# Kernel optimization log

Hardware: AMD Instinct MI355X
Metric: run time of the kernel (lower is better)

The kernel has to match this reference:

```python
import jax, jax.numpy as jnp
import numpy as np

N = 4096
H = 512
NUM_HEADS = 8
HEAD_DIM = H // NUM_HEADS
NUM_SETS = 1365


def setup_inputs() -> dict:
    key = jax.random.key(0)
    ks = jax.random.split(key, 24)
    s = 1.0 / np.sqrt(H)
    def lin(i):
        W = jax.random.normal(ks[i], (H, H), dtype=jnp.float32) * s
        b = jnp.zeros((H,), dtype=jnp.float32)
        return W, b
    Ws, bs = lin(0)
    Wq1, bq1 = lin(1); Wk1, bk1 = lin(2); Wv1, bv1 = lin(3); Wo1, bo1 = lin(4)
    Wq2, bq2 = lin(5); Wk2, bk2 = lin(6); Wv2, bv2 = lin(7); Wo2, bo2 = lin(8)
    # beta init is zeros in the module; use small nonzero so attention path matters
    beta1 = jnp.array([0.1], dtype=jnp.float32)
    beta2 = jnp.array([0.1], dtype=jnp.float32)
    embeddings = jax.random.normal(ks[9], (N, H), dtype=jnp.float32)
    batch_indices = jnp.sort(jax.random.randint(ks[10], (N,), 0, NUM_SETS))
    return dict(embeddings=embeddings, batch_indices=batch_indices,
                Ws=Ws, bs=bs,
                Wq1=Wq1, bq1=bq1, Wk1=Wk1, bk1=bk1, Wv1=Wv1, bv1=bv1, Wo1=Wo1, bo1=bo1, beta1=beta1,
                Wq2=Wq2, bq2=bq2, Wk2=Wk2, bk2=bk2, Wv2=Wv2, bv2=bv2, Wo2=Wo2, bo2=bo2, beta2=beta2)


def _attn_layer(x, mask, Wq, bq, Wk, bk, Wv, bv, Wo, bo, beta):
    n = x.shape[0]
    q = (x @ Wq + bq).reshape(n, NUM_HEADS, HEAD_DIM)
    k = (x @ Wk + bk).reshape(n, NUM_HEADS, HEAD_DIM)
    v = (x @ Wv + bv).reshape(n, NUM_HEADS, HEAD_DIM)
    scores = jnp.einsum('nhd,mhd->hnm', q, k) / np.sqrt(HEAD_DIM).astype(np.float32)
    scores = jnp.where(mask[None, :, :], scores, -jnp.inf)
    w = jax.nn.softmax(scores, axis=-1)
    w = jnp.nan_to_num(w, nan=0.0)  # rows with no valid key -> 0 (matches torch nan_to_num)
    out = jnp.einsum('hnm,mhd->nhd', w, v).reshape(n, H)
    return beta * (out @ Wo + bo) + x


def reference(embeddings, batch_indices, Ws, bs,
              Wq1, bq1, Wk1, bk1, Wv1, bv1, Wo1, bo1, beta1,
              Wq2, bq2, Wk2, bk2, Wv2, bv2, Wo2, bo2, beta2):
    n = embeddings.shape[0]
    static_emb = jax.nn.relu(embeddings @ Ws + bs)
    same_set = batch_indices[:, None] == batch_indices[None, :]
    mask = same_set & ~jnp.eye(n, dtype=bool)
    dyn = _attn_layer(embeddings, mask, Wq1, bq1, Wk1, bk1, Wv1, bv1, Wo1, bo1, beta1)
    dyn = _attn_layer(dyn, mask, Wq2, bq2, Wk2, bk2, Wv2, bv2, Wo2, bo2, beta2)
    sq = (dyn - static_emb) ** 2
    seg_sum = jax.ops.segment_sum(sq, batch_indices, num_segments=NUM_SETS)
    cnt = jax.ops.segment_sum(jnp.ones((n,), dtype=sq.dtype), batch_indices, num_segments=NUM_SETS)
    return seg_sum / jnp.maximum(cnt, 1.0)[:, None]
```

## Files before the change

kernel.cpp:

```cpp
#include <hip/hip_runtime.h>
#include <hip/hip_bf16.h>
#include <math.h>
#include <stdint.h>

#define N_NODES   4096
#define HDIM      512
#define NUM_HEADS 8
#define HEAD_DIM  64
#define NUM_SETS  1365
#define KDIM      512

typedef __attribute__((ext_vector_type(8))) short bf16x8;
typedef __attribute__((ext_vector_type(4))) float f32x4;

__device__ inline unsigned short f2bfu(float x) {
    __hip_bfloat16 h = __float2bfloat16(x);
    return __builtin_bit_cast(unsigned short, h);
}
__device__ inline float bfu2f(unsigned short u) {
    unsigned v = (unsigned)u << 16;
    return __builtin_bit_cast(float, v);
}

__device__ inline void gload_lds16(const void* g, void* l) {
    __builtin_amdgcn_global_load_lds(
        (const __attribute__((address_space(1))) unsigned int*)g,
        (__attribute__((address_space(3))) unsigned int*)l,
        16, 0, 0);
}

__global__ __launch_bounds__(256) void prep_kernel(
        const float* W0, const float* W1, const float* W2, const float* W3,
        const float* W4, const float* W5, const float* W6, const float* W7,
        const float* W8, __hip_bfloat16* __restrict__ wt,
        const float* __restrict__ emb, __hip_bfloat16* __restrict__ embb,
        const int* __restrict__ batch,
        int* __restrict__ seg_s, int* __restrict__ seg_e) {
    const int bx = blockIdx.x;
    if (bx < 2304) {
        __shared__ float t[32][36];
        const int z = bx >> 8;
        const int tb = bx & 255;
        const float* W = z==0?W0:z==1?W1:z==2?W2:z==3?W3:z==4?W4:z==5?W5:z==6?W6:z==7?W7:W8;
        __hip_bfloat16* Wt = wt + (size_t)z * (512 * 512);
        const int bn = (tb & 15) * 32, bk = (tb >> 4) * 32;
        const int nx = threadIdx.x & 7, ky = threadIdx.x >> 3;
        *(float4*)&t[ky][nx * 4] = *(const float4*)&W[(size_t)(bk + ky) * 512 + bn + nx * 4];
        __syncthreads();
        const int r2 = threadIdx.x >> 3;
        const int ck = threadIdx.x & 7;
        uint2 p;
        p.x = (unsigned)f2bfu(t[ck * 4 + 0][r2]) | ((unsigned)f2bfu(t[ck * 4 + 1][r2]) << 16);
        p.y = (unsigned)f2bfu(t[ck * 4 + 2][r2]) | ((unsigned)f2bfu(t[ck * 4 + 3][r2]) << 16);
        *(uint2*)&Wt[(size_t)(bn + r2) * 512 + bk + ck * 4] = p;
    } else if (bx < 4352) {
        const int i = (bx - 2304) * 256 + threadIdx.x;
        float4 v = ((const float4*)emb)[i];
        uint2 p;
        p.x = (unsigned)f2bfu(v.x) | ((unsigned)f2bfu(v.y) << 16);
        p.y = (unsigned)f2bfu(v.z) | ((unsigned)f2bfu(v.w) << 16);
        ((uint2*)embb)[i] = p;
    } else {
        const int i = (bx - 4352) * 256 + threadIdx.x;
        const int bi = batch[i];
        if (i == 0 || batch[i - 1] != bi) {
            int e = i + 1;
            while (e < N_NODES && batch[e] == bi) ++e;
            for (int j = i; j < e; ++j) { seg_s[j] = i; seg_e[j] = e; }
        }
    }
}

template<int MODE>
__global__ __launch_bounds__(512) void gemm128(
        const __hip_bfloat16* __restrict__ A,
        const __hip_bfloat16* __restrict__ Wt0, const __hip_bfloat16* __restrict__ Wt1,
        const __hip_bfloat16* __restrict__ Wt2, const __hip_bfloat16* __restrict__ Wt3,
        const float* __restrict__ bias0, const float* __restrict__ bias1,
        const float* __restrict__ bias2, const float* __restrict__ bias3,
        float* __restrict__ outF, __hip_bfloat16* __restrict__ outB) {
    __shared__ alignas(16) short Al[2][128][64];
    __shared__ alignas(16) short Bl[2][128][64];

    const int tid = threadIdx.x;
    const int wid = tid >> 6, lane = tid & 63;
    const int brow = blockIdx.x * 128;
    const int wsel = blockIdx.y >> 2;
    const int bcol = (blockIdx.y & 3) * 128;
    const __hip_bfloat16* Wt = (wsel == 0) ? Wt0 : (wsel == 1) ? Wt1 : (wsel == 2) ? Wt2 : Wt3;
    const float* bias        = (wsel == 0) ? bias0 : (wsel == 1) ? bias1 : (wsel == 2) ? bias2 : bias3;

    const int swzc = (lane & 7) ^ ((lane >> 3) & 7);
    const __hip_bfloat16* aSrc = A  + (size_t)(brow + wid * 16 + (lane >> 3)) * KDIM + swzc * 8;
    const __hip_bfloat16* bSrc = Wt + (size_t)(bcol + wid * 16 + (lane >> 3)) * KDIM + swzc * 8;

    const int fr = lane & 15, fq = lane >> 4;
    const int rx = fr & 7;
    const int wm = (wid >> 1) * 32;
    const int wn = (wid & 1) * 64;

    auto STAGE = [&](int buf, int t) {
        const int k0 = t * 64;
        gload_lds16(aSrc + k0, &Al[buf][wid * 16][0]);
        gload_lds16(aSrc + k0 + (size_t)8 * KDIM, &Al[buf][wid * 16 + 8][0]);
        gload_lds16(bSrc + k0, &Bl[buf][wid * 16][0]);
        gload_lds16(bSrc + k0 + (size_t)8 * KDIM, &Bl[buf][wid * 16 + 8][0]);
    };

    STAGE(0, 0);
    STAGE(1, 1);

    const int ch0 = ((0 + fq) ^ rx) * 8;
    const int ch1 = ((4 + fq) ^ rx) * 8;

    f32x4 acc[2][4] = {};
    #pragma unroll
    for (int t = 0; t < 8; ++t) {
        const int cur = t & 1;
        if (t < 7) asm volatile("s_waitcnt vmcnt(4)" ::: "memory");
        else       asm volatile("s_waitcnt vmcnt(0)" ::: "memory");
        __builtin_amdgcn_s_barrier();
        __builtin_amdgcn_sched_barrier(0);
        bf16x8 a0[2], a1[2], b0[4], b1[4];
        #pragma unroll
        for (int mi = 0; mi < 2; ++mi) {
            a0[mi] = *(const bf16x8*)&Al[cur][wm + mi * 16 + fr][ch0];
            a1[mi] = *(const bf16x8*)&Al[cur][wm + mi * 16 + fr][ch1];
        }
        #pragma unroll
        for (int ni = 0; ni < 4; ++ni) {
            b0[ni] = *(const bf16x8*)&Bl[cur][wn + ni * 16 + fr][ch0];
            b1[ni] = *(const bf16x8*)&Bl[cur][wn + ni * 16 + fr][ch1];
        }
        __builtin_amdgcn_s_setprio(1);
        #pragma unroll
        for (int mi = 0; mi < 2; ++mi)
            #pragma unroll
            for (int ni = 0; ni < 4; ++ni) {
                acc[mi][ni] = __builtin_amdgcn_mfma_f32_16x16x32_bf16(a0[mi], b0[ni], acc[mi][ni], 0, 0, 0);
                acc[mi][ni] = __builtin_amdgcn_mfma_f32_16x16x32_bf16(a1[mi], b1[ni], acc[mi][ni], 0, 0, 0);
            }
        __builtin_amdgcn_s_setprio(0);
        __builtin_amdgcn_sched_barrier(0);
        __builtin_amdgcn_s_barrier();
        if (t + 2 < 8) STAGE(cur, t + 2);
    }

    float bv[4];
    #pragma unroll
    for (int ni = 0; ni < 4; ++ni) bv[ni] = bias[bcol + wn + ni * 16 + fr];

    #pragma unroll
    for (int mi = 0; mi < 2; ++mi) {
        #pragma unroll
        for (int ni = 0; ni < 4; ++ni) {
            const int c = bcol + wn + ni * 16 + fr;
            #pragma unroll
            for (int r = 0; r < 4; ++r) {
                const int row = brow + wm + mi * 16 + fq * 4 + r;
                const float v = acc[mi][ni][r] + bv[ni];
                if (MODE == 0) {
                    if (wsel == 0) outF[(size_t)row * 512 + c] = fmaxf(v, 0.f);
                    else           outB[(size_t)row * 1536 + (wsel - 1) * 512 + c] = __float2bfloat16(v);
                } else {
                    outB[(size_t)row * 1536 + wsel * 512 + c] = __float2bfloat16(v);
                }
            }
        }
    }
}

__global__ __launch_bounds__(256) void gemm_oproj(
        const __hip_bfloat16* __restrict__ A, const __hip_bfloat16* __restrict__ Wt,
        const float* __restrict__ bias,
        float* __restrict__ outF, __hip_bfloat16* __restrict__ outB,
        const float* __restrict__ X, const float* __restrict__ betaP) {
    __shared__ alignas(16) short Al[2][64][64];
    __shared__ alignas(16) short Bl[2][64][64];

    const int tid = threadIdx.x;
    const int wid = tid >> 6, lane = tid & 63;
    const int brow = blockIdx.x * 64;
    const int bcol = blockIdx.y * 64;

    const int swzc = (lane & 7) ^ ((lane >> 3) & 7);
    const __hip_bfloat16* aSrc = A  + (size_t)(brow + wid * 16 + (lane >> 3)) * KDIM + swzc * 8;
    const __hip_bfloat16* bSrc = Wt + (size_t)(bcol + wid * 16 + (lane >> 3)) * KDIM + swzc * 8;

    const int fr = lane & 15, fq = lane >> 4;
    const int rx = fr & 7;
    const int wm = (wid >> 1) * 32, wn = (wid & 1) * 32;

    auto STAGE = [&](int buf, int t) {
        const int k0 = t * 64;
        gload_lds16(aSrc + k0, &Al[buf][wid * 16][0]);
        gload_lds16(aSrc + k0 + (size_t)8 * KDIM, &Al[buf][wid * 16 + 8][0]);
        gload_lds16(bSrc + k0, &Bl[buf][wid * 16][0]);
        gload_lds16(bSrc + k0 + (size_t)8 * KDIM, &Bl[buf][wid * 16 + 8][0]);
    };

    STAGE(0, 0);
    STAGE(1, 1);

    const int ch0 = ((0 + fq) ^ rx) * 8;
    const int ch1 = ((4 + fq) ^ rx) * 8;

    f32x4 acc[2][2] = {};
    #pragma unroll
    for (int t = 0; t < 8; ++t) {
        const int cur = t & 1;
        if (t < 7) asm volatile("s_waitcnt vmcnt(4)" ::: "memory");
        else       asm volatile("s_waitcnt vmcnt(0)" ::: "memory");
        __builtin_amdgcn_s_barrier();
        __builtin_amdgcn_sched_barrier(0);
        bf16x8 a0[2], a1[2], b0[2], b1[2];
        #pragma unroll
        for (int mi = 0; mi < 2; ++mi) {
            a0[mi] = *(const bf16x8*)&Al[cur][wm + mi * 16 + fr][ch0];
            a1[mi] = *(const bf16x8*)&Al[cur][wm + mi * 16 + fr][ch1];
        }
        #pragma unroll
        for (int ni = 0; ni < 2; ++ni) {
            b0[ni] = *(const bf16x8*)&Bl[cur][wn + ni * 16 + fr][ch0];
            b1[ni] = *(const bf16x8*)&Bl[cur][wn + ni * 16 + fr][ch1];
        }
        __builtin_amdgcn_s_setprio(1);
        #pragma unroll
        for (int mi = 0; mi < 2; ++mi)
            #pragma unroll
            for (int ni = 0; ni < 2; ++ni) {
                acc[mi][ni] = __builtin_amdgcn_mfma_f32_16x16x32_bf16(a0[mi], b0[ni], acc[mi][ni], 0, 0, 0);
                acc[mi][ni] = __builtin_amdgcn_mfma_f32_16x16x32_bf16(a1[mi], b1[ni], acc[mi][ni], 0, 0, 0);
            }
        __builtin_amdgcn_s_setprio(0);
        __builtin_amdgcn_sched_barrier(0);
        __builtin_amdgcn_s_barrier();
        if (t + 2 < 8) STAGE(cur, t + 2);
    }

    float bv[2];
    #pragma unroll
    for (int ni = 0; ni < 2; ++ni) bv[ni] = bias[bcol + wn + ni * 16 + fr];
    const float beta = betaP[0];
    const bool wb = (outB != nullptr);

    #pragma unroll
    for (int mi = 0; mi < 2; ++mi) {
        #pragma unroll
        for (int ni = 0; ni < 2; ++ni) {
            const int c = bcol + wn + ni * 16 + fr;
            #pragma unroll
            for (int r = 0; r < 4; ++r) {
                const int row = brow + wm + mi * 16 + fq * 4 + r;
                float v = beta * (acc[mi][ni][r] + bv[ni]) + X[(size_t)row * 512 + c];
                outF[(size_t)row * 512 + c] = v;
                if (wb) outB[(size_t)row * 512 + c] = __float2bfloat16(v);
            }
        }
    }
}

__global__ __launch_bounds__(256) void attn_kernel(
        const __hip_bfloat16* __restrict__ qkv,
        const int* __restrict__ seg_s, const int* __restrict__ seg_e,
        __hip_bfloat16* __restrict__ ab) {
    const int node = (blockIdx.x * blockDim.x + threadIdx.x) >> 6;
    const int lane = threadIdx.x & 63;
    const int c8   = lane * 8;

    bf16x8 q8 = *(const bf16x8*)&qkv[(size_t)node * 1536 + c8];
    float qf[8];
    #pragma unroll
    for (int j = 0; j < 8; ++j) qf[j] = bfu2f((unsigned short)q8[j]);

    const int s = seg_s[node], e = seg_e[node];

    float M = -INFINITY, S = 0.f;
    float o[8] = {};
    for (int m = s; m < e; ++m) {
        if (m == node) continue;
        bf16x8 k8 = *(const bf16x8*)&qkv[(size_t)m * 1536 + 512 + c8];
        float p = 0.f;
        #pragma unroll
        for (int j = 0; j < 8; ++j) p = fmaf(qf[j], bfu2f((unsigned short)k8[j]), p);
        p += __shfl_xor(p, 1, 64);
        p += __shfl_xor(p, 2, 64);
        p += __shfl_xor(p, 4, 64);
        const float sc = p * 0.125f;
        const float newM = fmaxf(M, sc);
        const float scale = __expf(M - newM);
        const float w = __expf(sc - newM);
        S = S * scale + w;
        bf16x8 v8 = *(const bf16x8*)&qkv[(size_t)m * 1536 + 1024 + c8];
        #pragma unroll
        for (int j = 0; j < 8; ++j) o[j] = fmaf(w, bfu2f((unsigned short)v8[j]), o[j] * scale);
        M = newM;
    }
    const float inv = (S > 0.f) ? (1.f / S) : 0.f;
    bf16x8 r;
    #pragma unroll
    for (int j = 0; j < 8; ++j) r[j] = (short)f2bfu(o[j] * inv);
    *(bf16x8*)&ab[(size_t)node * 512 + c8] = r;
}

__global__ __launch_bounds__(256) void seg_mse_kernel(
        const float* __restrict__ dyn, const float* __restrict__ stat,
        const int* __restrict__ batch, float* __restrict__ out) {
    const int s = blockIdx.x;
    const int d = threadIdx.x * 2;
    int lo = 0, hi = N_NODES;
    while (lo < hi) { int m = (lo + hi) >> 1; if (batch[m] < s) lo = m + 1; else hi = m; }
    const int a = lo;
    hi = N_NODES;
    while (lo < hi) { int m = (lo + hi) >> 1; if (batch[m] <= s) lo = m + 1; else hi = m; }
    const int b = lo;

    float acc0 = 0.f, acc1 = 0.f;
    for (int i = a; i < b; ++i) {
        const float2 dv = *(const float2*)&dyn[(size_t)i * 512 + d];
        const float2 sv = *(const float2*)&stat[(size_t)i * 512 + d];
        const float d0 = dv.x - sv.x, d1 = dv.y - sv.y;
        acc0 += d0 * d0; acc1 += d1 * d1;
    }
    const float inv = 1.f / fmaxf((float)(b - a), 1.f);
    float2 r; r.x = acc0 * inv; r.y = acc1 * inv;
    *(float2*)&out[(size_t)s * 512 + d] = r;
}

extern "C" void kernel_launch(void* const* d_in, const int* in_sizes, int n_in,
                              void* d_out, int out_size, void* d_ws, size_t ws_size,
                              hipStream_t stream) {
    const float* emb   = (const float*)d_in[0];
    const int*   batch = (const int*)  d_in[1];
    const float* Ws_   = (const float*)d_in[2];
    const float* bs_   = (const float*)d_in[3];
    const float* Wq1 = (const float*)d_in[4];  const float* bq1 = (const float*)d_in[5];
    const float* Wk1 = (const float*)d_in[6];  const float* bk1 = (const float*)d_in[7];
    const float* Wv1 = (const float*)d_in[8];  const float* bv1 = (const float*)d_in[9];
    const float* Wo1 = (const float*)d_in[10]; const float* bo1 = (const float*)d_in[11];
    const float* beta1 = (const float*)d_in[12];
    const float* Wq2 = (const float*)d_in[13]; const float* bq2 = (const float*)d_in[14];
    const float* Wk2 = (const float*)d_in[15]; const float* bk2 = (const float*)d_in[16];
    const float* Wv2 = (const float*)d_in[17]; const float* bv2 = (const float*)d_in[18];
    const float* Wo2 = (const float*)d_in[19]; const float* bo2 = (const float*)d_in[20];
    const float* beta2 = (const float*)d_in[21];

    char* w = (char*)d_ws;
    const size_t MB = 1024 * 1024;
    float* stat            = (float*)(w + 0 * MB);
    float* dyn             = (float*)(w + 8 * MB);
    __hip_bfloat16* qkv    = (__hip_bfloat16*)(w + 16 * MB);
    float* dyn2            = (float*)(w + 16 * MB);
    __hip_bfloat16* embb   = (__hip_bfloat16*)(w + 28 * MB);
    __hip_bfloat16* ab     = (__hip_bfloat16*)(w + 32 * MB);
    __hip_bfloat16* dynb   = (__hip_bfloat16*)(w + 36 * MB);
    __hip_bfloat16* wt     = (__hip_bfloat16*)(w + 40 * MB);
    int* seg_s = (int*)(w + 45 * MB);
    int* seg_e = seg_s + N_NODES;

    const size_t WSZ = 512 * 512;
    __hip_bfloat16* wtS  = wt + 0 * WSZ;
    __hip_bfloat16* wtQ1 = wt + 1 * WSZ;
    __hip_bfloat16* wtK1 = wt + 2 * WSZ;
    __hip_bfloat16* wtV1 = wt + 3 * WSZ;
    __hip_bfloat16* wtO1 = wt + 4 * WSZ;
    __hip_bfloat16* wtQ2 = wt + 5 * WSZ;
    __hip_bfloat16* wtK2 = wt + 6 * WSZ;
    __hip_bfloat16* wtV2 = wt + 7 * WSZ;
    __hip_bfloat16* wtO2 = wt + 8 * WSZ;

    prep_kernel<<<4368, 256, 0, stream>>>(
        Ws_, Wq1, Wk1, Wv1, Wo1, Wq2, Wk2, Wv2, Wo2, wt,
        emb, embb, batch, seg_s, seg_e);

    gemm128<0><<<dim3(32, 16), 512, 0, stream>>>(
        embb, wtS, wtQ1, wtK1, wtV1, bs_, bq1, bk1, bv1, stat, qkv);
    attn_kernel<<<N_NODES / 4, 256, 0, stream>>>(qkv, seg_s, seg_e, ab);
    gemm_oproj<<<dim3(64, 8), 256, 0, stream>>>(ab, wtO1, bo1, dyn, dynb, emb, beta1);

    gemm128<1><<<dim3(32, 12), 512, 0, stream>>>(
        dynb, wtQ2, wtK2, wtV2, wtV2, bq2, bk2, bv2, bv2, nullptr, qkv);
    attn_kernel<<<N_NODES / 4, 256, 0, stream>>>(qkv, seg_s, seg_e, ab);
    gemm_oproj<<<dim3(64, 8), 256, 0, stream>>>(ab, wtO2, bo2, dyn2, nullptr, dyn, beta2);

    seg_mse_kernel<<<NUM_SETS, 256, 0, stream>>>(dyn2, stat, batch, (float*)d_out);
}
```

Before: 84.27 us.

## Enlarge per-wave GEMM tiles and halve thread counts in projection kernels

The QKV GEMM keeps its 128x128 block tile but now uses 4 waves instead of 8, so each wave computes a 64x64 sub-tile with 16 accumulators and issues 8 async loads per stage. The output-projection GEMM widens its block tile to 64x128 and launches half as many blocks. The goal is more MFMA work per LDS fragment read and fewer blocks and barriers. In exchange there is more register pressure, less latency hiding per CU, and fewer blocks to fill the GPU.

Result: slower. 93.77 us (+11.3%).

```diff
diff --git a/kernel.cpp b/kernel.cpp
--- a/kernel.cpp
+++ b/kernel.cpp
@@ -72,7 +72,7 @@
 }
 
 template<int MODE>
-__global__ __launch_bounds__(512) void gemm128(
+__global__ __launch_bounds__(256) void gemm128(
         const __hip_bfloat16* __restrict__ A,
         const __hip_bfloat16* __restrict__ Wt0, const __hip_bfloat16* __restrict__ Wt1,
         const __hip_bfloat16* __restrict__ Wt2, const __hip_bfloat16* __restrict__ Wt3,
@@ -91,56 +91,52 @@
     const float* bias        = (wsel == 0) ? bias0 : (wsel == 1) ? bias1 : (wsel == 2) ? bias2 : bias3;
 
     const int swzc = (lane & 7) ^ ((lane >> 3) & 7);
-    const __hip_bfloat16* aSrc = A  + (size_t)(brow + wid * 16 + (lane >> 3)) * KDIM + swzc * 8;
-    const __hip_bfloat16* bSrc = Wt + (size_t)(bcol + wid * 16 + (lane >> 3)) * KDIM + swzc * 8;
+    const __hip_bfloat16* aSrc = A  + (size_t)(brow + wid * 32 + (lane >> 3)) * KDIM + swzc * 8;
+    const __hip_bfloat16* bSrc = Wt + (size_t)(bcol + wid * 32 + (lane >> 3)) * KDIM + swzc * 8;
 
     const int fr = lane & 15, fq = lane >> 4;
     const int rx = fr & 7;
-    const int wm = (wid >> 1) * 32;
+    const int wm = (wid >> 1) * 64;
     const int wn = (wid & 1) * 64;
 
     auto STAGE = [&](int buf, int t) {
         const int k0 = t * 64;
-        gload_lds16(aSrc + k0, &Al[buf][wid * 16][0]);
-        gload_lds16(aSrc + k0 + (size_t)8 * KDIM, &Al[buf][wid * 16 + 8][0]);
-        gload_lds16(bSrc + k0, &Bl[buf][wid * 16][0]);
-        gload_lds16(bSrc + k0 + (size_t)8 * KDIM, &Bl[buf][wid * 16 + 8][0]);
+        #pragma unroll
+        for (int i = 0; i < 4; ++i) {
+            gload_lds16(aSrc + k0 + (size_t)(i * 8) * KDIM, &Al[buf][wid * 32 + i * 8][0]);
+            gload_lds16(bSrc + k0 + (size_t)(i * 8) * KDIM, &Bl[buf][wid * 32 + i * 8][0]);
+        }
     };
 
     STAGE(0, 0);
     STAGE(1, 1);
 
-    const int ch0 = ((0 + fq) ^ rx) * 8;
-    const int ch1 = ((4 + fq) ^ rx) * 8;
-
-    f32x4 acc[2][4] = {};
+    f32x4 acc[4][4] = {};
     #pragma unroll
     for (int t = 0; t < 8; ++t) {
         const int cur = t & 1;
-        if (t < 7) asm volatile("s_waitcnt vmcnt(4)" ::: "memory");
+        if (t < 7) asm volatile("s_waitcnt vmcnt(8)" ::: "memory");
         else       asm volatile("s_waitcnt vmcnt(0)" ::: "memory");
         __builtin_amdgcn_s_barrier();
         __builtin_amdgcn_sched_barrier(0);
-        bf16x8 a0[2], a1[2], b0[4], b1[4];
-        #pragma unroll
-        for (int mi = 0; mi < 2; ++mi) {
-            a0[mi] = *(const bf16x8*)&Al[cur][wm + mi * 16 + fr][ch0];
-            a1[mi] = *(const bf16x8*)&Al[cur][wm + mi * 16 + fr][ch1];
-        }
-        #pragma unroll
-        for (int ni = 0; ni < 4; ++ni) {
-            b0[ni] = *(const bf16x8*)&Bl[cur][wn + ni * 16 + fr][ch0];
-            b1[ni] = *(const bf16x8*)&Bl[cur][wn + ni * 16 + fr][ch1];
-        }
-        __builtin_amdgcn_s_setprio(1);
-        #pragma unroll
-        for (int mi = 0; mi < 2; ++mi)
-            #pragma unroll
-            for (int ni = 0; ni < 4; ++ni) {
-                acc[mi][ni] = __builtin_amdgcn_mfma_f32_16x16x32_bf16(a0[mi], b0[ni], acc[mi][ni], 0, 0, 0);
-                acc[mi][ni] = __builtin_amdgcn_mfma_f32_16x16x32_bf16(a1[mi], b1[ni], acc[mi][ni], 0, 0, 0);
-            }
-        __builtin_amdgcn_s_setprio(0);
+        #pragma unroll
+        for (int kk = 0; kk < 2; ++kk) {
+            const int ch = ((kk * 4 + fq) ^ rx) * 8;
+            bf16x8 af[4], bfv[4];
+            #pragma unroll
+            for (int mi = 0; mi < 4; ++mi)
+                af[mi] = *(const bf16x8*)&Al[cur][wm + mi * 16 + fr][ch];
+            #pragma unroll
+            for (int ni = 0; ni < 4; ++ni)
+                bfv[ni] = *(const bf16x8*)&Bl[cur][wn + ni * 16 + fr][ch];
+            __builtin_amdgcn_s_setprio(1);
+            #pragma unroll
+            for (int mi = 0; mi < 4; ++mi)
+                #pragma unroll
+                for (int ni = 0; ni < 4; ++ni)
+                    acc[mi][ni] = __builtin_amdgcn_mfma_f32_16x16x32_bf16(af[mi], bfv[ni], acc[mi][ni], 0, 0, 0);
+            __builtin_amdgcn_s_setprio(0);
+        }
         __builtin_amdgcn_sched_barrier(0);
         __builtin_amdgcn_s_barrier();
         if (t + 2 < 8) STAGE(cur, t + 2);
@@ -151,7 +147,7 @@
     for (int ni = 0; ni < 4; ++ni) bv[ni] = bias[bcol + wn + ni * 16 + fr];
 
     #pragma unroll
-    for (int mi = 0; mi < 2; ++mi) {
+    for (int mi = 0; mi < 4; ++mi) {
         #pragma unroll
         for (int ni = 0; ni < 4; ++ni) {
             const int c = bcol + wn + ni * 16 + fr;
@@ -176,78 +172,76 @@
         float* __restrict__ outF, __hip_bfloat16* __restrict__ outB,
         const float* __restrict__ X, const float* __restrict__ betaP) {
     __shared__ alignas(16) short Al[2][64][64];
-    __shared__ alignas(16) short Bl[2][64][64];
+    __shared__ alignas(16) short Bl[2][128][64];
 
     const int tid = threadIdx.x;
     const int wid = tid >> 6, lane = tid & 63;
     const int brow = blockIdx.x * 64;
-    const int bcol = blockIdx.y * 64;
+    const int bcol = blockIdx.y * 128;
 
     const int swzc = (lane & 7) ^ ((lane >> 3) & 7);
     const __hip_bfloat16* aSrc = A  + (size_t)(brow + wid * 16 + (lane >> 3)) * KDIM + swzc * 8;
-    const __hip_bfloat16* bSrc = Wt + (size_t)(bcol + wid * 16 + (lane >> 3)) * KDIM + swzc * 8;
+    const __hip_bfloat16* bSrc = Wt + (size_t)(bcol + wid * 32 + (lane >> 3)) * KDIM + swzc * 8;
 
     const int fr = lane & 15, fq = lane >> 4;
     const int rx = fr & 7;
-    const int wm = (wid >> 1) * 32, wn = (wid & 1) * 32;
+    const int wm = (wid >> 1) * 32;
+    const int wn = (wid & 1) * 64;
 
     auto STAGE = [&](int buf, int t) {
         const int k0 = t * 64;
-        gload_lds16(aSrc + k0, &Al[buf][wid * 16][0]);
-        gload_lds16(aSrc + k0 + (size_t)8 * KDIM, &Al[buf][wid * 16 + 8][0]);
-        gload_lds16(bSrc + k0, &Bl[buf][wid * 16][0]);
-        gload_lds16(bSrc + k0 + (size_t)8 * KDIM, &Bl[buf][wid * 16 + 8][0]);
+        #pragma unroll
+        for (int i = 0; i < 2; ++i)
+            gload_lds16(aSrc + k0 + (size_t)(i * 8) * KDIM, &Al[buf][wid * 16 + i * 8][0]);
+        #pragma unroll
+        for (int i = 0; i < 4; ++i)
+            gload_lds16(bSrc + k0 + (size_t)(i * 8) * KDIM, &Bl[buf][wid * 32 + i * 8][0]);
     };
 
     STAGE(0, 0);
     STAGE(1, 1);
 
-    const int ch0 = ((0 + fq) ^ rx) * 8;
-    const int ch1 = ((4 + fq) ^ rx) * 8;
-
-    f32x4 acc[2][2] = {};
+    f32x4 acc[2][4] = {};
     #pragma unroll
     for (int t = 0; t < 8; ++t) {
         const int cur = t & 1;
-        if (t < 7) asm volatile("s_waitcnt vmcnt(4)" ::: "memory");
+        if (t < 7) asm volatile("s_waitcnt vmcnt(6)" ::: "memory");
         else       asm volatile("s_waitcnt vmcnt(0)" ::: "memory");
         __builtin_amdgcn_s_barrier();
         __builtin_amdgcn_sched_barrier(0);
-        bf16x8 a0[2], a1[2], b0[2], b1[2];
-        #pragma unroll
-        for (int mi = 0; mi < 2; ++mi) {
-            a0[mi] = *(const bf16x8*)&Al[cur][wm + mi * 16 + fr][ch0];
-            a1[mi] = *(const bf16x8*)&Al[cur][wm + mi * 16 + fr][ch1];
-        }
-        #pragma unroll
-        for (int ni = 0; ni < 2; ++ni) {
-            b0[ni] = *(const bf16x8*)&Bl[cur][wn + ni * 16 + fr][ch0];
-            b1[ni] = *(const bf16x8*)&Bl[cur][wn + ni * 16 + fr][ch1];
-        }
-        __builtin_amdgcn_s_setprio(1);
-        #pragma unroll
-        for (int mi = 0; mi < 2; ++mi)
-            #pragma unroll
-            for (int ni = 0; ni < 2; ++ni) {
-                acc[mi][ni] = __builtin_amdgcn_mfma_f32_16x16x32_bf16(a0[mi], b0[ni], acc[mi][ni], 0, 0, 0);
-                acc[mi][ni] = __builtin_amdgcn_mfma_f32_16x16x32_bf16(a1[mi], b1[ni], acc[mi][ni], 0, 0, 0);
-            }
-        __builtin_amdgcn_s_setprio(0);
+        #pragma unroll
+        for (int kk = 0; kk < 2; ++kk) {
+            const int ch = ((kk * 4 + fq) ^ rx) * 8;
+            bf16x8 af[2], bfv[4];
+            #pragma unroll
+            for (int mi = 0; mi < 2; ++mi)
+                af[mi] = *(const bf16x8*)&Al[cur][wm + mi * 16 + fr][ch];
+            #pragma unroll
+            for (int ni = 0; ni < 4; ++ni)
+                bfv[ni] = *(const bf16x8*)&Bl[cur][wn + ni * 16 + fr][ch];
+            __builtin_amdgcn_s_setprio(1);
+            #pragma unroll
+            for (int mi = 0; mi < 2; ++mi)
+                #pragma unroll
+                for (int ni = 0; ni < 4; ++ni)
+                    acc[mi][ni] = __builtin_amdgcn_mfma_f32_16x16x32_bf16(af[mi], bfv[ni], acc[mi][ni], 0, 0, 0);
+            __builtin_amdgcn_s_setprio(0);
+        }
         __builtin_amdgcn_sched_barrier(0);
         __builtin_amdgcn_s_barrier();
         if (t + 2 < 8) STAGE(cur, t + 2);
     }
 
-    float bv[2];
-    #pragma unroll
-    for (int ni = 0; ni < 2; ++ni) bv[ni] = bias[bcol + wn + ni * 16 + fr];
+    float bv[4];
+    #pragma unroll
+    for (int ni = 0; ni < 4; ++ni) bv[ni] = bias[bcol + wn + ni * 16 + fr];
     const float beta = betaP[0];
     const bool wb = (outB != nullptr);
 
     #pragma unroll
     for (int mi = 0; mi < 2; ++mi) {
         #pragma unroll
-        for (int ni = 0; ni < 2; ++ni) {
+        for (int ni = 0; ni < 4; ++ni) {
             const int c = bcol + wn + ni * 16 + fr;
             #pragma unroll
             for (int r = 0; r < 4; ++r) {
@@ -373,15 +367,15 @@
         Ws_, Wq1, Wk1, Wv1, Wo1, Wq2, Wk2, Wv2, Wo2, wt,
         emb, embb, batch, seg_s, seg_e);
 
-    gemm128<0><<<dim3(32, 16), 512, 0, stream>>>(
+    gemm128<0><<<dim3(32, 16), 256, 0, stream>>>(
         embb, wtS, wtQ1, wtK1, wtV1, bs_, bq1, bk1, bv1, stat, qkv);
     attn_kernel<<<N_NODES / 4, 256, 0, stream>>>(qkv, seg_s, seg_e, ab);
-    gemm_oproj<<<dim3(64, 8), 256, 0, stream>>>(ab, wtO1, bo1, dyn, dynb, emb, beta1);
-
-    gemm128<1><<<dim3(32, 12), 512, 0, stream>>>(
+    gemm_oproj<<<dim3(64, 4), 256, 0, stream>>>(ab, wtO1, bo1, dyn, dynb, emb, beta1);
+
+    gemm128<1><<<dim3(32, 12), 256, 0, stream>>>(
         dynb, wtQ2, wtK2, wtV2, wtV2, bq2, bk2, bv2, bv2, nullptr, qkv);
     attn_kernel<<<N_NODES / 4, 256, 0, stream>>>(qkv, seg_s, seg_e, ab);
-    gemm_oproj<<<dim3(64, 8), 256, 0, stream>>>(ab, wtO2, bo2, dyn2, nullptr, dyn, beta2);
+    gemm_oproj<<<dim3(64, 4), 256, 0, stream>>>(ab, wtO2, bo2, dyn2, nullptr, dyn, beta2);
 
     seg_mse_kernel<<<NUM_SETS, 256, 0, stream>>>(dyn2, stat, batch, (float*)d_out);
 }
```
